# Performance work log

Hardware: AMD Instinct MI355X
Metric: run time of the kernel (lower is better)

## Reference

```python
import jax, jax.numpy as jnp
import numpy as np
from jax import lax

B, T, D, H = 4096, 256, 18, 32


def setup_inputs() -> dict:
    key = jax.random.key(0)
    ks = jax.random.split(key, 9)
    s = 1.0 / np.sqrt(H)  # PyTorch LSTM init scale
    return {
        "batch": jax.random.normal(ks[0], (B, T, D), dtype=jnp.float32),
        "W_ih": jax.random.normal(ks[1], (4 * H, D), dtype=jnp.float32) * s,
        "W_hh": jax.random.normal(ks[2], (4 * H, H), dtype=jnp.float32) * s,
        "b_ih": jax.random.normal(ks[3], (4 * H,), dtype=jnp.float32) * s,
        "b_hh": jax.random.normal(ks[4], (4 * H,), dtype=jnp.float32) * s,
        "W1": jax.random.normal(ks[5], (512, H * T), dtype=jnp.float32) * 0.02,
        "b1": jax.random.normal(ks[6], (512,), dtype=jnp.float32) * 0.02,
        "W2": jax.random.normal(ks[7], (1, 512), dtype=jnp.float32) * 0.02,
        "b2": jax.random.normal(ks[8], (1,), dtype=jnp.float32) * 0.02,
    }


def _lstm(batch, W_ih, W_hh, b_ih, b_hh):
    b, t, _ = batch.shape
    h = batch.dtype.type
    # Precompute input projections for all timesteps: [B, T, 4H]
    x_proj = jnp.einsum('bti,gi->btg', batch, W_ih) + b_ih + b_hh
    W_hh_T = W_hh.T  # [H, 4H]

    def step(carry, xp):
        h_prev, c_prev = carry
        gates = xp + h_prev @ W_hh_T  # [B, 4H]
        i, f, g, o = jnp.split(gates, 4, axis=-1)  # PyTorch gate order i,f,g,o
        i = jax.nn.sigmoid(i)
        f = jax.nn.sigmoid(f)
        g = jnp.tanh(g)
        o = jax.nn.sigmoid(o)
        c = f * c_prev + i * g
        h_new = o * jnp.tanh(c)
        return (h_new, c), h_new

    h0 = jnp.zeros((b, H), dtype=batch.dtype)
    c0 = jnp.zeros((b, H), dtype=batch.dtype)
    _, hs = lax.scan(step, (h0, c0), x_proj.transpose(1, 0, 2))  # hs: [T, B, H]
    return hs.transpose(1, 0, 2)  # [B, T, H]


def reference(batch, W_ih, W_hh, b_ih, b_hh, W1, b1, W2, b2):
    hs = _lstm(batch, W_ih, W_hh, b_ih, b_hh)            # [B, T, H]
    flat = hs.reshape(hs.shape[0], -1)                   # [B, T*H]
    hid = jax.nn.relu(flat @ W1.T + b1)                  # [B, 512]
    return hid @ W2.T + b2                               # [B, 1]
```

## Files before the change

### kernel.cpp

```cpp
#include <hip/hip_runtime.h>
#include <hip/hip_bf16.h>
#include <stdint.h>

typedef float f32x4 __attribute__((ext_vector_type(4)));
typedef _Float16 half8 __attribute__((ext_vector_type(8)));
typedef _Float16 half2_ __attribute__((ext_vector_type(2)));

#define B_ 4096
#define T_ 256
#define D_ 18
#define H_ 32
#define GK 8192
#define GN 512
#define KSPLIT 4
#define SLOT 520

__device__ __forceinline__ float fsig(float x) {
  float e = __builtin_amdgcn_exp2f(-1.442695041f * x);
  return __builtin_amdgcn_rcpf(1.0f + e);
}
__device__ __forceinline__ float ftanh(float x) {
  float e = __builtin_amdgcn_exp2f(-2.885390082f * x);
  return 2.0f * __builtin_amdgcn_rcpf(1.0f + e) - 1.0f;
}
__device__ __forceinline__ void ldsbar() {
  asm volatile("s_waitcnt lgkmcnt(0)\n\ts_barrier" ::: "memory");
}

__global__ __launch_bounds__(256) void cvtw1_kernel(const float* __restrict__ w1,
                                                    unsigned short* __restrict__ dst) {
  int i = blockIdx.x * 256 + threadIdx.x;
  float4 v = ((const float4*)w1)[i];
  unsigned short a = __builtin_bit_cast(unsigned short, (_Float16)v.x);
  unsigned short b = __builtin_bit_cast(unsigned short, (_Float16)v.y);
  unsigned short c = __builtin_bit_cast(unsigned short, (_Float16)v.z);
  unsigned short d = __builtin_bit_cast(unsigned short, (_Float16)v.w);
  uint2 o; o.x = (unsigned)a | ((unsigned)b << 16); o.y = (unsigned)c | ((unsigned)d << 16);
  ((uint2*)dst)[i] = o;
}

__global__ __launch_bounds__(512) void lstm_kernel(
    const float* __restrict__ batch, const float* __restrict__ W_ih,
    const float* __restrict__ W_hh, const float* __restrict__ b_ih,
    const float* __restrict__ b_hh, _Float16* __restrict__ hs) {
  __shared__ _Float16 hist[8 * SLOT];
  __shared__ _Float16 xs[2 * 4096];

  const int tid = (int)threadIdx.x;
  const int lane = tid & 63;
  const int w = tid >> 6;
  const int lq = lane >> 4;
  const int lr = lane & 15;
  const int b0 = (int)blockIdx.x * 16;

  half8 wx, wh;
  {
    int grow = (lr & 3) * 32 + w * 4 + (lr >> 2);
#pragma unroll
    for (int j = 0; j < 8; ++j) {
      int k = lq * 8 + j;
      wx[j] = (k < D_) ? (_Float16)W_ih[grow * D_ + k] : (_Float16)0.0f;
      wh[j] = (_Float16)W_hh[grow * H_ + k];
    }
  }
  f32x4 bias4;
#pragma unroll
  for (int r = 0; r < 4; ++r) {
    int g = r * 32 + w * 4 + lq;
    bias4[r] = b_ih[g] + b_hh[g];
  }

  const int rdo = lr * 32 + ((lq ^ ((lr >> 1) & 3)) << 3);
  const int kcol = w * 4 + lq;
  const int wro = lr * 32 + ((((kcol >> 3) ^ ((lr >> 1) & 3))) << 3) + (kcol & 7);

  const int fe = tid >> 5;
  const int fs = (tid >> 2) & 7;
  const int fg = tid & 3;
  const int fl_rd = fs * SLOT + fe * 32 + ((fg ^ ((fe >> 1) & 3)) << 3);
  _Float16* fl_wp = hs + (size_t)(b0 + fe) * GK + fs * H_ + fg * 8;

  const int e0 = tid / 36, q0 = tid - e0 * 36;
  const int i1 = tid + 512;
  const int e1 = i1 / 36, q1 = i1 - e1 * 36;
  const float* xld0 = batch + (size_t)(b0 + e0) * (T_ * D_) + q0 * 4;
  const float* xld1 = batch + (size_t)(b0 + e1) * (T_ * D_) + q1 * 4;
  float4 xv0, xv1;

#define XLOAD(tb)                                                              \
  do {                                                                         \
    xv0 = *(const float4*)(xld0 + (tb) * 144);                                 \
    if (tid < 64) xv1 = *(const float4*)(xld1 + (tb) * 144);                   \
  } while (0)

#define XPUT(E, Q, V, buf)                                                     \
  do {                                                                         \
    int swz_ = ((E) >> 1) & 3;                                                 \
    _Pragma("unroll") for (int j = 0; j < 4; ++j) {                            \
      int f_ = (Q) * 4 + j;                                                    \
      int to_ = (f_ * 57) >> 10;                          \
      int d_ = f_ - to_ * 18;                                                  \
      float val_ = (j == 0) ? (V).x : (j == 1) ? (V).y : (j == 2) ? (V).z : (V).w; \
      xs[(buf) * 4096 + to_ * 512 + (E) * 32 + (((d_ >> 3) ^ swz_) << 3) + (d_ & 7)] = \
          (_Float16)val_;                                                      \
    }                                                                          \
  } while (0)

#define XSTORE(buf)                                                            \
  do {                                                                         \
    XPUT(e0, q0, xv0, buf);                                                    \
    if (tid < 64) XPUT(e1, q1, xv1, buf);                                      \
  } while (0)

#define STEP(tt, xo)                                                           \
  do {                                                                         \
    half8 hf = *(const half8*)&hist[(((tt) + 7) & 7) * SLOT + rdo];            \
    half8 xf = *(const half8*)&xs[(xo) + (tt) * 512 + rdo];                    \
    f32x4 acc = bias4;                                                         \
    acc = __builtin_amdgcn_mfma_f32_16x16x32_f16(wx, xf, acc, 0, 0, 0);        \
    acc = __builtin_amdgcn_mfma_f32_16x16x32_f16(wh, hf, acc, 0, 0, 0);        \
    float iv = fsig(acc[0]);                                                   \
    float fv = fsig(acc[1]);                                                   \
    float gv = ftanh(acc[2]);                                                  \
    float ov = fsig(acc[3]);                                                   \
    c = fmaf(fv, c, iv * gv);                                                  \
    float h = ov * ftanh(c);                                                   \
    hist[((tt) & 7) * SLOT + wro] = (_Float16)h;                               \
    ldsbar();                                                                  \
  } while (0)

  XLOAD(0);
  for (int i = tid; i < 8 * SLOT; i += 512) hist[i] = (_Float16)0.0f;
  for (int i = tid; i < 8192; i += 512) xs[i] = (_Float16)0.0f;
  ldsbar();
  XSTORE(0);
  XLOAD(1);
  ldsbar();

  float c = 0.0f;
  for (int blk = 0; blk < 32; ++blk) {
    const int xo = (blk & 1) * 4096;
    STEP(0, xo); STEP(1, xo); STEP(2, xo); STEP(3, xo);
    STEP(4, xo); STEP(5, xo); STEP(6, xo); STEP(7, xo);
    half8 hv = *(const half8*)&hist[fl_rd];
    *(half8*)(fl_wp + blk * 8 * H_) = hv;
    if (blk < 31) XSTORE((blk & 1) ^ 1);
    if (blk < 30) XLOAD(blk + 2);
    ldsbar();
  }
#undef STEP
#undef XSTORE
#undef XPUT
#undef XLOAD
}

__global__ __launch_bounds__(256, 2) void gemm_kernel(
    const _Float16* __restrict__ Ahs, const _Float16* __restrict__ Bw1,
    float* __restrict__ part) {
  __shared__ _Float16 As[2 * 128 * 64];
  __shared__ _Float16 Bs[2 * 128 * 64];

  const int bid = (int)blockIdx.x;
  const int m0 = (bid & 31) << 7;
  const int n0 = ((bid >> 5) & 3) << 7;
  const int ksp = bid >> 7;
  const int k0 = ksp << 11;
  float* outp = part + (size_t)ksp * ((size_t)B_ * GN);

  const int tid = (int)threadIdx.x;
  const int lane = tid & 63, w = tid >> 6;
  const int wm = w & 1, wn = w >> 1;
  const int lq = lane >> 4, lr = lane & 15;

  const _Float16* gA[4]; const _Float16* gB[4]; int lp[4];
#pragma unroll
  for (int j = 0; j < 4; ++j) {
    int p = tid + 256 * j;
    int row = p >> 3, q = p & 7, cg = q ^ (row & 7);
    gA[j] = Ahs + (size_t)(m0 + row) * GK + k0 + cg * 8;
    gB[j] = Bw1 + (size_t)(n0 + row) * GK + k0 + cg * 8;
    lp[j] = p * 8;
  }

  int offA[4][2], offB[4][2];
#pragma unroll
  for (int mt = 0; mt < 4; ++mt)
#pragma unroll
    for (int ks = 0; ks < 2; ++ks) {
      int m = wm * 64 + mt * 16 + lr;
      offA[mt][ks] = m * 64 + (((lq + ks * 4) ^ (m & 7)) << 3);
      int n = wn * 64 + mt * 16 + lr;
      offB[mt][ks] = n * 64 + (((lq + ks * 4) ^ (n & 7)) << 3);
    }

  f32x4 acc[4][4];
#pragma unroll
  for (int mt = 0; mt < 4; ++mt)
#pragma unroll
    for (int nt = 0; nt < 4; ++nt) {
      acc[mt][nt][0] = 0.f; acc[mt][nt][1] = 0.f;
      acc[mt][nt][2] = 0.f; acc[mt][nt][3] = 0.f;
    }

  half8 va0[4], vb0[4], va1[4], vb1[4];
#pragma unroll
  for (int j = 0; j < 4; ++j) {
    va0[j] = *(const half8*)gA[j];        vb0[j] = *(const half8*)gB[j];
    va1[j] = *(const half8*)(gA[j] + 64); vb1[j] = *(const half8*)(gB[j] + 64);
    gA[j] += 128; gB[j] += 128;
  }

#define GPHASE(SET, POFF, guard)                                               \
  do {                                                                         \
    _Pragma("unroll") for (int j = 0; j < 4; ++j) {                            \
      *(half8*)&As[(POFF) + lp[j]] = va##SET[j];                               \
      *(half8*)&Bs[(POFF) + lp[j]] = vb##SET[j];                               \
    }                                                                          \
    if (guard) {                                                               \
      _Pragma("unroll") for (int j = 0; j < 4; ++j) {                          \
        va##SET[j] = *(const half8*)gA[j];                                     \
        vb##SET[j] = *(const half8*)gB[j];                                     \
        gA[j] += 64; gB[j] += 64;                                              \
      }                                                                        \
    }                                                                          \
    ldsbar();                                                                  \
    half8 af[4][2], bf[4][2];                                                  \
    _Pragma("unroll") for (int mt = 0; mt < 4; ++mt)                           \
      _Pragma("unroll") for (int ks = 0; ks < 2; ++ks) {                       \
        af[mt][ks] = *(const half8*)&As[(POFF) + offA[mt][ks]];                \
        bf[mt][ks] = *(const half8*)&Bs[(POFF) + offB[mt][ks]];                \
      }                                                                        \
    _Pragma("unroll") for (int ks = 0; ks < 2; ++ks)                           \
      _Pragma("unroll") for (int mt = 0; mt < 4; ++mt)                         \
        _Pragma("unroll") for (int nt = 0; nt < 4; ++nt)                       \
          acc[mt][nt] = __builtin_amdgcn_mfma_f32_16x16x32_f16(                \
              af[mt][ks], bf[nt][ks], acc[mt][nt], 0, 0, 0);                   \
  } while (0)

  for (int it2 = 0; it2 < 16; ++it2) {
    const bool g = (it2 < 15);
    GPHASE(0, 0, g);
    GPHASE(1, 8192, g);
  }
#undef GPHASE

#pragma unroll
  for (int mt = 0; mt < 4; ++mt)
#pragma unroll
    for (int nt = 0; nt < 4; ++nt) {
      int n = n0 + wn * 64 + nt * 16 + lr;
#pragma unroll
      for (int r = 0; r < 4; ++r) {
        int m = m0 + wm * 64 + mt * 16 + lq * 4 + r;
        outp[(size_t)m * GN + n] = acc[mt][nt][r];
      }
    }
}

__global__ __launch_bounds__(256) void head_kernel(const float* __restrict__ part,
                                                   const float* __restrict__ b1,
                                                   const float* __restrict__ W2,
                                                   const float* __restrict__ b2,
                                                   float* __restrict__ out) {
  const int b = (int)(blockIdx.x * 4 + (threadIdx.x >> 6));
  const int l = (int)(threadIdx.x & 63);
  const size_t stride = (size_t)B_ * GN;
  const float4* b14 = (const float4*)b1;
  const float4* w4 = (const float4*)W2;
  float s = 0.0f;
#pragma unroll
  for (int p = 0; p < 2; ++p) {
    int i = p * 64 + l;
    float4 hv = ((const float4*)(part + (size_t)b * GN))[i];
#pragma unroll
    for (int sp = 1; sp < KSPLIT; ++sp) {
      float4 pv = ((const float4*)(part + sp * stride + (size_t)b * GN))[i];
      hv.x += pv.x; hv.y += pv.y; hv.z += pv.z; hv.w += pv.w;
    }
    float4 bv = b14[i], wv = w4[i];
    float t0 = fmaxf(hv.x + bv.x, 0.0f);
    float t1 = fmaxf(hv.y + bv.y, 0.0f);
    float t2 = fmaxf(hv.z + bv.z, 0.0f);
    float t3 = fmaxf(hv.w + bv.w, 0.0f);
    s = fmaf(t0, wv.x, s); s = fmaf(t1, wv.y, s);
    s = fmaf(t2, wv.z, s); s = fmaf(t3, wv.w, s);
  }
#pragma unroll
  for (int off = 32; off >= 1; off >>= 1) s += __shfl_xor(s, off);
  if (l == 0) out[b] = s + b2[0];
}

extern "C" void kernel_launch(void* const* d_in, const int* in_sizes, int n_in,
                              void* d_out, int out_size, void* d_ws, size_t ws_size,
                              hipStream_t stream) {
  const float* batch = (const float*)d_in[0];
  const float* W_ih = (const float*)d_in[1];
  const float* W_hh = (const float*)d_in[2];
  const float* b_ih = (const float*)d_in[3];
  const float* b_hh = (const float*)d_in[4];
  const float* W1 = (const float*)d_in[5];
  const float* b1 = (const float*)d_in[6];
  const float* W2 = (const float*)d_in[7];
  const float* b2 = (const float*)d_in[8];
  float* out = (float*)d_out;

  char* ws = (char*)d_ws;
  _Float16* hs = (_Float16*)ws;
  _Float16* w1h = (_Float16*)(ws + 67108864);
  float* part = (float*)(ws + 67108864 + 8388608);

  cvtw1_kernel<<<4096, 256, 0, stream>>>(W1, (unsigned short*)w1h);
  lstm_kernel<<<256, 512, 0, stream>>>(batch, W_ih, W_hh, b_ih, b_hh, hs);
  gemm_kernel<<<512, 256, 0, stream>>>(hs, w1h, part);
  head_kernel<<<1024, 256, 0, stream>>>(part, b1, W2, b2, out);
}
```

Before: 256.0 us.

## Double-buffer LSTM h history and pipeline input-projection MFMAs across timesteps

Doubles the hidden-state history buffer in LDS to two 8-slot halves. This removes the per-block extra barrier and lets the flush of the previous block's h values, along with the x staging stores and loads, be interleaved into the middle of the next block. The input-projection MFMA for step t+1 is issued while step t's gate math runs, taking it off the serial recurrence critical path. The gate math is also fused so that sigmoid(i)*tanh(g) and sigmoid(o)*tanh(c) each use a single reciprocal, cutting transcendental count. It costs more LDS and register pressure, and the changed rounding order may shift numerics slightly.

New measurement: 233.8 us. -8.7%, faster.

```diff
diff --git a/kernel.cpp b/kernel.cpp
--- a/kernel.cpp
+++ b/kernel.cpp
@@ -4,7 +4,6 @@
 
 typedef float f32x4 __attribute__((ext_vector_type(4)));
 typedef _Float16 half8 __attribute__((ext_vector_type(8)));
-typedef _Float16 half2_ __attribute__((ext_vector_type(2)));
 
 #define B_ 4096
 #define T_ 256
@@ -18,10 +17,6 @@
 __device__ __forceinline__ float fsig(float x) {
   float e = __builtin_amdgcn_exp2f(-1.442695041f * x);
   return __builtin_amdgcn_rcpf(1.0f + e);
-}
-__device__ __forceinline__ float ftanh(float x) {
-  float e = __builtin_amdgcn_exp2f(-2.885390082f * x);
-  return 2.0f * __builtin_amdgcn_rcpf(1.0f + e) - 1.0f;
 }
 __device__ __forceinline__ void ldsbar() {
   asm volatile("s_waitcnt lgkmcnt(0)\n\ts_barrier" ::: "memory");
@@ -43,7 +38,7 @@
     const float* __restrict__ batch, const float* __restrict__ W_ih,
     const float* __restrict__ W_hh, const float* __restrict__ b_ih,
     const float* __restrict__ b_hh, _Float16* __restrict__ hs) {
-  __shared__ _Float16 hist[8 * SLOT];
+  __shared__ _Float16 hist[16 * SLOT];
   __shared__ _Float16 xs[2 * 4096];
 
   const int tid = (int)threadIdx.x;
@@ -112,25 +107,28 @@
     if (tid < 64) XPUT(e1, q1, xv1, buf);                                      \
   } while (0)
 
-#define STEP(tt, xo)                                                           \
-  do {                                                                         \
-    half8 hf = *(const half8*)&hist[(((tt) + 7) & 7) * SLOT + rdo];            \
-    half8 xf = *(const half8*)&xs[(xo) + (tt) * 512 + rdo];                    \
-    f32x4 acc = bias4;                                                         \
-    acc = __builtin_amdgcn_mfma_f32_16x16x32_f16(wx, xf, acc, 0, 0, 0);        \
-    acc = __builtin_amdgcn_mfma_f32_16x16x32_f16(wh, hf, acc, 0, 0, 0);        \
-    float iv = fsig(acc[0]);                                                   \
+#define STEP(tt, AXC, PRE)                                                     \
+  do {                                                                         \
+    _Float16* hrd = ((tt) == 0 ? po + 7 * SLOT : pr + ((tt)-1) * SLOT);        \
+    half8 hf = *(const half8*)&hrd[rdo];                                       \
+    f32x4 acc = __builtin_amdgcn_mfma_f32_16x16x32_f16(wh, hf, AXC, 0, 0, 0);  \
+    PRE;                                                                       \
+    float ei = __builtin_amdgcn_exp2f(-1.442695041f * acc[0]);                 \
+    float eg = __builtin_amdgcn_exp2f(-2.885390082f * acc[2]);                 \
+    float ig = (1.0f - eg) *                                                   \
+               __builtin_amdgcn_rcpf((1.0f + ei) * (1.0f + eg));               \
     float fv = fsig(acc[1]);                                                   \
-    float gv = ftanh(acc[2]);                                                  \
-    float ov = fsig(acc[3]);                                                   \
-    c = fmaf(fv, c, iv * gv);                                                  \
-    float h = ov * ftanh(c);                                                   \
-    hist[((tt) & 7) * SLOT + wro] = (_Float16)h;                               \
+    c = fmaf(fv, c, ig);                                                       \
+    float eo = __builtin_amdgcn_exp2f(-1.442695041f * acc[3]);                 \
+    float ec = __builtin_amdgcn_exp2f(-2.885390082f * c);                      \
+    float h = (1.0f - ec) *                                                    \
+              __builtin_amdgcn_rcpf((1.0f + eo) * (1.0f + ec));                \
+    pr[(tt)*SLOT + wro] = (_Float16)h;                                         \
     ldsbar();                                                                  \
   } while (0)
 
   XLOAD(0);
-  for (int i = tid; i < 8 * SLOT; i += 512) hist[i] = (_Float16)0.0f;
+  for (int i = tid; i < 16 * SLOT; i += 512) hist[i] = (_Float16)0.0f;
   for (int i = tid; i < 8192; i += 512) xs[i] = (_Float16)0.0f;
   ldsbar();
   XSTORE(0);
@@ -139,14 +137,35 @@
 
   float c = 0.0f;
   for (int blk = 0; blk < 32; ++blk) {
-    const int xo = (blk & 1) * 4096;
-    STEP(0, xo); STEP(1, xo); STEP(2, xo); STEP(3, xo);
-    STEP(4, xo); STEP(5, xo); STEP(6, xo); STEP(7, xo);
-    half8 hv = *(const half8*)&hist[fl_rd];
-    *(half8*)(fl_wp + blk * 8 * H_) = hv;
-    if (blk < 31) XSTORE((blk & 1) ^ 1);
+    const int p = blk & 1;
+    _Float16* pr = hist + p * (8 * SLOT);
+    _Float16* po = hist + (p ^ 1) * (8 * SLOT);
+    const int xo = p * 4096;
+
+    half8 xq[8];
+#pragma unroll
+    for (int j = 0; j < 8; ++j) xq[j] = *(const half8*)&xs[xo + j * 512 + rdo];
+    f32x4 ax0, ax1;
+    ax0 = __builtin_amdgcn_mfma_f32_16x16x32_f16(wx, xq[0], bias4, 0, 0, 0);
+
+    STEP(0, ax0, ax1 = __builtin_amdgcn_mfma_f32_16x16x32_f16(wx, xq[1], bias4, 0, 0, 0));
+    STEP(1, ax1, ax0 = __builtin_amdgcn_mfma_f32_16x16x32_f16(wx, xq[2], bias4, 0, 0, 0));
+    STEP(2, ax0, ax1 = __builtin_amdgcn_mfma_f32_16x16x32_f16(wx, xq[3], bias4, 0, 0, 0));
+    STEP(3, ax1, ax0 = __builtin_amdgcn_mfma_f32_16x16x32_f16(wx, xq[4], bias4, 0, 0, 0));
+    if (blk < 31) XSTORE(p ^ 1);
     if (blk < 30) XLOAD(blk + 2);
-    ldsbar();
+    STEP(4, ax0, ax1 = __builtin_amdgcn_mfma_f32_16x16x32_f16(wx, xq[5], bias4, 0, 0, 0));
+    if (blk) {
+      half8 hv = *(const half8*)&hist[(p ^ 1) * (8 * SLOT) + fl_rd];
+      *(half8*)(fl_wp + (size_t)(blk - 1) * (8 * H_)) = hv;
+    }
+    STEP(5, ax1, ax0 = __builtin_amdgcn_mfma_f32_16x16x32_f16(wx, xq[6], bias4, 0, 0, 0));
+    STEP(6, ax0, ax1 = __builtin_amdgcn_mfma_f32_16x16x32_f16(wx, xq[7], bias4, 0, 0, 0));
+    STEP(7, ax1, );
+  }
+  {
+    half8 hv = *(const half8*)&hist[8 * SLOT + fl_rd];
+    *(half8*)(fl_wp + (size_t)31 * (8 * H_)) = hv;
   }
 #undef STEP
 #undef XSTORE
```
